# Kernel optimization log

Hardware: AMD Instinct MI355X
Metric: run time of the kernel (lower is better)

The kernel has to match this reference:

```python
import jax, jax.numpy as jnp
import numpy as np

M_CHECKS = 256      # check nodes
DC = 16             # variables per check (check degree)
NEURONS = M_CHECKS * DC  # 4096 Tanner-graph edges
BATCH = 1024
EPS = 1e-8


def build_mask():
    # edge id = check*DC + t ; mask[j, i] = 1 iff same check, different variable
    block = np.ones((DC, DC), np.float32) - np.eye(DC, dtype=np.float32)
    return jnp.asarray(np.kron(np.eye(M_CHECKS, dtype=np.float32), block))


def setup_inputs() -> dict:
    key = jax.random.key(0)
    k1, k2 = jax.random.split(key)
    # tanh-domain variable-to-check messages, |x| < ~1 (keeps exp(sum log|x|) stable)
    x = 0.25 * jax.random.normal(k1, (BATCH, NEURONS), dtype=jnp.float32)
    mask = build_mask()
    # learned weights initialized near 1 (weighted-BP init)
    even_weights = 1.0 + 0.02 * jax.random.normal(k2, (NEURONS, NEURONS), dtype=jnp.float32)
    return {"x": x, "even_weights": even_weights, "w_even2odd_mask": mask}


def reference(x, even_weights, w_even2odd_mask):
    log_abs_x = jnp.log(jnp.abs(x) + EPS)                       # [B, E]
    x_b = 0.5 - 0.5 * jnp.sign(x)                               # hard bits
    syndrome = jnp.mod(x_b @ w_even2odd_mask, 2.0)              # [B, E]
    bipolar_syndrome = 1.0 - 2.0 * syndrome
    log_abs_x_tanner = log_abs_x @ (w_even2odd_mask * even_weights)
    even_prod_messages = bipolar_syndrome * jnp.exp(log_abs_x_tanner)
    return jnp.log((1.0 + even_prod_messages + EPS) / (1.0 - even_prod_messages + EPS))
```

## Files before the change

kernel.cpp:

```cpp
#include <hip/hip_runtime.h>


constexpr int M_CHECKS = 256;
constexpr int DC = 16;
constexpr int NEURONS = M_CHECKS * DC;
constexpr int BATCH = 1024;
constexpr float EPS = 1e-8f;

constexpr int CB = 16;
constexpr int BB = 16;
constexpr int BS4 = 65;

__global__ __launch_bounds__(256) void even_layer_kernel(
    const float* __restrict__ x,
    const float* __restrict__ w,
    float* __restrict__ out)
{
    __shared__ float4 Wsh[CB * BS4];

    const int tid = (int)threadIdx.x;
    const int cb  = (int)blockIdx.x & 15;
    const int bb  = (int)blockIdx.x >> 4;

    {
        const int cl = tid >> 4;
        const int j  = tid & 15;
        const int c  = cb * CB + cl;
        const float* src = w + (size_t)(c * DC + j) * NEURONS + (size_t)(c * DC);
        #pragma unroll
        for (int k = 0; k < 4; ++k) {
            float4 v = *(const float4*)(src + 4 * k);
            if ((j >> 2) == k) {
                if ((j & 3) == 0) v.x = 0.0f;
                else if ((j & 3) == 1) v.y = 0.0f;
                else if ((j & 3) == 2) v.z = 0.0f;
                else v.w = 0.0f;
            }
            Wsh[cl * BS4 + j * 4 + k] = v;
        }
    }
    __syncthreads();

    const int bi = tid >> 4;
    const int ci = tid & 15;
    const int b  = bb * BB + bi;
    const int c  = cb * CB + ci;

    const float* xp = x + (size_t)b * NEURONS + (size_t)(c * DC);

    float la[DC];
    int sbits = 0;

    #define LOADPROC(XV, J)                                   \
        { const float xv_ = (XV);                             \
          la[J] = logf(fabsf(xv_) + EPS);                     \
          if (xv_ < 0.0f) sbits |= (1 << (J)); }

    #pragma unroll
    for (int k = 0; k < 4; ++k) {
        const float4 v = *(const float4*)(xp + 4 * k);
        LOADPROC(v.x, 4 * k + 0)
        LOADPROC(v.y, 4 * k + 1)
        LOADPROC(v.z, 4 * k + 2)
        LOADPROC(v.w, 4 * k + 3)
    }
    const int sall = __popc(sbits) & 1;

    float acc[DC];
    #pragma unroll
    for (int i = 0; i < DC; ++i) acc[i] = 0.0f;

    const int wbase = ci * BS4;
    #pragma unroll
    for (int j = 0; j < DC; ++j) {
        const float lj = la[j];
        const float4 w0 = Wsh[wbase + j * 4 + 0];
        const float4 w1 = Wsh[wbase + j * 4 + 1];
        const float4 w2 = Wsh[wbase + j * 4 + 2];
        const float4 w3 = Wsh[wbase + j * 4 + 3];
        acc[0]  = fmaf(lj, w0.x, acc[0]);
        acc[1]  = fmaf(lj, w0.y, acc[1]);
        acc[2]  = fmaf(lj, w0.z, acc[2]);
        acc[3]  = fmaf(lj, w0.w, acc[3]);
        acc[4]  = fmaf(lj, w1.x, acc[4]);
        acc[5]  = fmaf(lj, w1.y, acc[5]);
        acc[6]  = fmaf(lj, w1.z, acc[6]);
        acc[7]  = fmaf(lj, w1.w, acc[7]);
        acc[8]  = fmaf(lj, w2.x, acc[8]);
        acc[9]  = fmaf(lj, w2.y, acc[9]);
        acc[10] = fmaf(lj, w2.z, acc[10]);
        acc[11] = fmaf(lj, w2.w, acc[11]);
        acc[12] = fmaf(lj, w3.x, acc[12]);
        acc[13] = fmaf(lj, w3.y, acc[13]);
        acc[14] = fmaf(lj, w3.z, acc[14]);
        acc[15] = fmaf(lj, w3.w, acc[15]);
    }

    float* op = out + (size_t)b * NEURONS + (size_t)(c * DC);

    #define EPI(RCOMP, I)                                                   \
        { const float e_ = expf(acc[I]);                                    \
          const int par_ = sall ^ ((sbits >> (I)) & 1);                     \
          const float even_ = par_ ? -e_ : e_;                              \
          RCOMP = logf((1.0f + even_ + EPS) / (1.0f - even_ + EPS)); }

    #pragma unroll
    for (int k = 0; k < 4; ++k) {
        float4 r;
        EPI(r.x, 4 * k + 0)
        EPI(r.y, 4 * k + 1)
        EPI(r.z, 4 * k + 2)
        EPI(r.w, 4 * k + 3)
        *(float4*)(op + 4 * k) = r;
    }

    #undef LOADPROC
    #undef EPI
}

extern "C" void kernel_launch(void* const* d_in, const int* in_sizes, int n_in,
                              void* d_out, int out_size, void* d_ws, size_t ws_size,
                              hipStream_t stream) {
    const float* x = (const float*)d_in[0];
    const float* w = (const float*)d_in[1];
    float* out = (float*)d_out;

    dim3 grid((BATCH / BB) * (M_CHECKS / CB));
    dim3 block(256);
    hipLaunchKernelGGL(even_layer_kernel, grid, block, 0, stream, x, w, out);
}
```

Before: 17.81 us.

## Split each check-batch task across two threads with shared log-magnitude staging

```diff
diff --git a/kernel.cpp b/kernel.cpp
--- a/kernel.cpp
+++ b/kernel.cpp
@@ -8,104 +8,98 @@
 constexpr float EPS = 1e-8f;
 
 constexpr int CB = 16;
-constexpr int BB = 16;
+constexpr int BB = 8;
+constexpr int TASKS = CB * BB;
 constexpr int BS4 = 65;
 
-__global__ __launch_bounds__(256) void even_layer_kernel(
+__global__ __launch_bounds__(256, 6) void even_layer_kernel(
     const float* __restrict__ x,
     const float* __restrict__ w,
     float* __restrict__ out)
 {
     __shared__ float4 Wsh[CB * BS4];
+    __shared__ float  la_t[DC][TASKS + 1];
+    __shared__ int    msk_sh[2][TASKS + 2];
 
     const int tid = (int)threadIdx.x;
     const int cb  = (int)blockIdx.x & 15;
     const int bb  = (int)blockIdx.x >> 4;
 
+    const int task = tid >> 1;
+    const int h    = tid & 1;
+    const int bi   = task >> 4;
+    const int ci   = task & 15;
+    const int b    = bb * BB + bi;
+    const int c    = cb * CB + ci;
+
+    const float* xp = x + (size_t)b * NEURONS + (size_t)(c * DC + h * 8);
+    const float4 v0 = *(const float4*)(xp);
+    const float4 v1 = *(const float4*)(xp + 4);
+
     {
         const int cl = tid >> 4;
         const int j  = tid & 15;
-        const int c  = cb * CB + cl;
-        const float* src = w + (size_t)(c * DC + j) * NEURONS + (size_t)(c * DC);
+        const int cc = cb * CB + cl;
+        const float* src = w + (size_t)(cc * DC + j) * NEURONS + (size_t)(cc * DC);
         #pragma unroll
         for (int k = 0; k < 4; ++k) {
-            float4 v = *(const float4*)(src + 4 * k);
+            float4 wv = *(const float4*)(src + 4 * k);
             if ((j >> 2) == k) {
-                if ((j & 3) == 0) v.x = 0.0f;
-                else if ((j & 3) == 1) v.y = 0.0f;
-                else if ((j & 3) == 2) v.z = 0.0f;
-                else v.w = 0.0f;
+                if ((j & 3) == 0) wv.x = 0.0f;
+                else if ((j & 3) == 1) wv.y = 0.0f;
+                else if ((j & 3) == 2) wv.z = 0.0f;
+                else wv.w = 0.0f;
             }
-            Wsh[cl * BS4 + j * 4 + k] = v;
+            Wsh[cl * BS4 + j * 4 + k] = wv;
         }
+    }
+
+    {
+        const float xv[8] = {v0.x, v0.y, v0.z, v0.w, v1.x, v1.y, v1.z, v1.w};
+        int m8 = 0;
+        #pragma unroll
+        for (int jj = 0; jj < 8; ++jj) {
+            const float lv = logf(fabsf(xv[jj]) + EPS);
+            if (xv[jj] < 0.0f) m8 |= (1 << jj);
+            la_t[h * 8 + jj][task] = lv;
+        }
+        msk_sh[h][task] = m8;
     }
     __syncthreads();
 
-    const int bi = tid >> 4;
-    const int ci = tid & 15;
-    const int b  = bb * BB + bi;
-    const int c  = cb * CB + ci;
+    const int sbits = msk_sh[0][task] | (msk_sh[1][task] << 8);
+    const int sall  = __popc(sbits) & 1;
 
-    const float* xp = x + (size_t)b * NEURONS + (size_t)(c * DC);
+    float acc[8];
+    #pragma unroll
+    for (int i = 0; i < 8; ++i) acc[i] = 0.0f;
 
-    float la[DC];
-    int sbits = 0;
-
-    #define LOADPROC(XV, J)                                   \
-        { const float xv_ = (XV);                             \
-          la[J] = logf(fabsf(xv_) + EPS);                     \
-          if (xv_ < 0.0f) sbits |= (1 << (J)); }
-
-    #pragma unroll
-    for (int k = 0; k < 4; ++k) {
-        const float4 v = *(const float4*)(xp + 4 * k);
-        LOADPROC(v.x, 4 * k + 0)
-        LOADPROC(v.y, 4 * k + 1)
-        LOADPROC(v.z, 4 * k + 2)
-        LOADPROC(v.w, 4 * k + 3)
-    }
-    const int sall = __popc(sbits) & 1;
-
-    float acc[DC];
-    #pragma unroll
-    for (int i = 0; i < DC; ++i) acc[i] = 0.0f;
-
-    const int wbase = ci * BS4;
+    const int wbase = ci * BS4 + h * 2;
     #pragma unroll
     for (int j = 0; j < DC; ++j) {
-        const float lj = la[j];
-        const float4 w0 = Wsh[wbase + j * 4 + 0];
-        const float4 w1 = Wsh[wbase + j * 4 + 1];
-        const float4 w2 = Wsh[wbase + j * 4 + 2];
-        const float4 w3 = Wsh[wbase + j * 4 + 3];
-        acc[0]  = fmaf(lj, w0.x, acc[0]);
-        acc[1]  = fmaf(lj, w0.y, acc[1]);
-        acc[2]  = fmaf(lj, w0.z, acc[2]);
-        acc[3]  = fmaf(lj, w0.w, acc[3]);
-        acc[4]  = fmaf(lj, w1.x, acc[4]);
-        acc[5]  = fmaf(lj, w1.y, acc[5]);
-        acc[6]  = fmaf(lj, w1.z, acc[6]);
-        acc[7]  = fmaf(lj, w1.w, acc[7]);
-        acc[8]  = fmaf(lj, w2.x, acc[8]);
-        acc[9]  = fmaf(lj, w2.y, acc[9]);
-        acc[10] = fmaf(lj, w2.z, acc[10]);
-        acc[11] = fmaf(lj, w2.w, acc[11]);
-        acc[12] = fmaf(lj, w3.x, acc[12]);
-        acc[13] = fmaf(lj, w3.y, acc[13]);
-        acc[14] = fmaf(lj, w3.z, acc[14]);
-        acc[15] = fmaf(lj, w3.w, acc[15]);
+        const float lj = la_t[j][task];
+        const float4 wlo = Wsh[wbase + j * 4];
+        const float4 whi = Wsh[wbase + j * 4 + 1];
+        acc[0] = fmaf(lj, wlo.x, acc[0]);
+        acc[1] = fmaf(lj, wlo.y, acc[1]);
+        acc[2] = fmaf(lj, wlo.z, acc[2]);
+        acc[3] = fmaf(lj, wlo.w, acc[3]);
+        acc[4] = fmaf(lj, whi.x, acc[4]);
+        acc[5] = fmaf(lj, whi.y, acc[5]);
+        acc[6] = fmaf(lj, whi.z, acc[6]);
+        acc[7] = fmaf(lj, whi.w, acc[7]);
     }
 
-    float* op = out + (size_t)b * NEURONS + (size_t)(c * DC);
+    float* op = out + (size_t)b * NEURONS + (size_t)(c * DC + h * 8);
 
     #define EPI(RCOMP, I)                                                   \
         { const float e_ = expf(acc[I]);                                    \
-          const int par_ = sall ^ ((sbits >> (I)) & 1);                     \
+          const int par_ = sall ^ ((sbits >> (h * 8 + (I))) & 1);           \
           const float even_ = par_ ? -e_ : e_;                              \
           RCOMP = logf((1.0f + even_ + EPS) / (1.0f - even_ + EPS)); }
 
     #pragma unroll
-    for (int k = 0; k < 4; ++k) {
+    for (int k = 0; k < 2; ++k) {
         float4 r;
         EPI(r.x, 4 * k + 0)
         EPI(r.y, 4 * k + 1)
@@ -113,8 +107,6 @@
         EPI(r.w, 4 * k + 3)
         *(float4*)(op + 4 * k) = r;
     }
-
-    #undef LOADPROC
     #undef EPI
 }
 
@@ -126,6 +118,6 @@
     float* out = (float*)d_out;
 
     dim3 grid((BATCH / BB) * (M_CHECKS / CB));
-    dim3 block(256);
+    dim3 block(2 * TASKS);
     hipLaunchKernelGGL(even_layer_kernel, grid, block, 0, stream, x, w, out);
 }
```

After: 19.10 us. 1.07x slower.

## Process two batch tiles per block and prefetch x before weight staging

Applied to the files above, without the earlier changes.

```diff
diff --git a/kernel.cpp b/kernel.cpp
--- a/kernel.cpp
+++ b/kernel.cpp
@@ -9,75 +9,24 @@
 
 constexpr int CB = 16;
 constexpr int BB = 16;
+constexpr int SETS = 2;
 constexpr int BS4 = 65;
 
-__global__ __launch_bounds__(256) void even_layer_kernel(
-    const float* __restrict__ x,
-    const float* __restrict__ w,
-    float* __restrict__ out)
+__device__ __forceinline__ void matvec_epi_store(
+    const float4* __restrict__ wrow,
+    const float la[DC], const int sbits, float* __restrict__ op)
 {
-    __shared__ float4 Wsh[CB * BS4];
-
-    const int tid = (int)threadIdx.x;
-    const int cb  = (int)blockIdx.x & 15;
-    const int bb  = (int)blockIdx.x >> 4;
-
-    {
-        const int cl = tid >> 4;
-        const int j  = tid & 15;
-        const int c  = cb * CB + cl;
-        const float* src = w + (size_t)(c * DC + j) * NEURONS + (size_t)(c * DC);
-        #pragma unroll
-        for (int k = 0; k < 4; ++k) {
-            float4 v = *(const float4*)(src + 4 * k);
-            if ((j >> 2) == k) {
-                if ((j & 3) == 0) v.x = 0.0f;
-                else if ((j & 3) == 1) v.y = 0.0f;
-                else if ((j & 3) == 2) v.z = 0.0f;
-                else v.w = 0.0f;
-            }
-            Wsh[cl * BS4 + j * 4 + k] = v;
-        }
-    }
-    __syncthreads();
-
-    const int bi = tid >> 4;
-    const int ci = tid & 15;
-    const int b  = bb * BB + bi;
-    const int c  = cb * CB + ci;
-
-    const float* xp = x + (size_t)b * NEURONS + (size_t)(c * DC);
-
-    float la[DC];
-    int sbits = 0;
-
-    #define LOADPROC(XV, J)                                   \
-        { const float xv_ = (XV);                             \
-          la[J] = logf(fabsf(xv_) + EPS);                     \
-          if (xv_ < 0.0f) sbits |= (1 << (J)); }
-
-    #pragma unroll
-    for (int k = 0; k < 4; ++k) {
-        const float4 v = *(const float4*)(xp + 4 * k);
-        LOADPROC(v.x, 4 * k + 0)
-        LOADPROC(v.y, 4 * k + 1)
-        LOADPROC(v.z, 4 * k + 2)
-        LOADPROC(v.w, 4 * k + 3)
-    }
-    const int sall = __popc(sbits) & 1;
-
     float acc[DC];
     #pragma unroll
     for (int i = 0; i < DC; ++i) acc[i] = 0.0f;
 
-    const int wbase = ci * BS4;
     #pragma unroll
     for (int j = 0; j < DC; ++j) {
         const float lj = la[j];
-        const float4 w0 = Wsh[wbase + j * 4 + 0];
-        const float4 w1 = Wsh[wbase + j * 4 + 1];
-        const float4 w2 = Wsh[wbase + j * 4 + 2];
-        const float4 w3 = Wsh[wbase + j * 4 + 3];
+        const float4 w0 = wrow[j * 4 + 0];
+        const float4 w1 = wrow[j * 4 + 1];
+        const float4 w2 = wrow[j * 4 + 2];
+        const float4 w3 = wrow[j * 4 + 3];
         acc[0]  = fmaf(lj, w0.x, acc[0]);
         acc[1]  = fmaf(lj, w0.y, acc[1]);
         acc[2]  = fmaf(lj, w0.z, acc[2]);
@@ -96,7 +45,7 @@
         acc[15] = fmaf(lj, w3.w, acc[15]);
     }
 
-    float* op = out + (size_t)b * NEURONS + (size_t)(c * DC);
+    const int sall = __popc(sbits) & 1;
 
     #define EPI(RCOMP, I)                                                   \
         { const float e_ = expf(acc[I]);                                    \
@@ -113,9 +62,85 @@
         EPI(r.w, 4 * k + 3)
         *(float4*)(op + 4 * k) = r;
     }
+    #undef EPI
+}
 
-    #undef LOADPROC
-    #undef EPI
+__device__ __forceinline__ void log_abs_pack(
+    const float4 xv[4], float la[DC], int& sbits)
+{
+    const float xs[16] = {xv[0].x, xv[0].y, xv[0].z, xv[0].w,
+                          xv[1].x, xv[1].y, xv[1].z, xv[1].w,
+                          xv[2].x, xv[2].y, xv[2].z, xv[2].w,
+                          xv[3].x, xv[3].y, xv[3].z, xv[3].w};
+    sbits = 0;
+    #pragma unroll
+    for (int j = 0; j < DC; ++j) {
+        la[j] = logf(fabsf(xs[j]) + EPS);
+        if (xs[j] < 0.0f) sbits |= (1 << j);
+    }
+}
+
+__global__ __launch_bounds__(256) void even_layer_kernel(
+    const float* __restrict__ x,
+    const float* __restrict__ w,
+    float* __restrict__ out)
+{
+    __shared__ float4 Wsh[CB * BS4];
+
+    const int tid = (int)threadIdx.x;
+    const int cb  = (int)blockIdx.x & 15;
+    const int bg  = (int)blockIdx.x >> 4;
+
+    const int bi = tid >> 4;
+    const int ci = tid & 15;
+    const int b0 = bg * (SETS * BB) + bi;
+    const int b1 = b0 + BB;
+    const int c  = cb * CB + ci;
+
+    const float* xp0 = x + (size_t)b0 * NEURONS + (size_t)(c * DC);
+    const float* xp1 = x + (size_t)b1 * NEURONS + (size_t)(c * DC);
+
+    float4 xv0[4];
+    #pragma unroll
+    for (int k = 0; k < 4; ++k) xv0[k] = *(const float4*)(xp0 + 4 * k);
+
+    const int cl = tid >> 4;
+    const int jr = tid & 15;
+    const int cc = cb * CB + cl;
+    const float* wsrc = w + (size_t)(cc * DC + jr) * NEURONS + (size_t)(cc * DC);
+    float4 wreg[4];
+    #pragma unroll
+    for (int k = 0; k < 4; ++k) wreg[k] = *(const float4*)(wsrc + 4 * k);
+
+    float la0[DC]; int sb0;
+    log_abs_pack(xv0, la0, sb0);
+
+    #pragma unroll
+    for (int k = 0; k < 4; ++k) {
+        float4 wv = wreg[k];
+        if ((jr >> 2) == k) {
+            if ((jr & 3) == 0) wv.x = 0.0f;
+            else if ((jr & 3) == 1) wv.y = 0.0f;
+            else if ((jr & 3) == 2) wv.z = 0.0f;
+            else wv.w = 0.0f;
+        }
+        Wsh[cl * BS4 + jr * 4 + k] = wv;
+    }
+
+    float4 xv1[4];
+    #pragma unroll
+    for (int k = 0; k < 4; ++k) xv1[k] = *(const float4*)(xp1 + 4 * k);
+
+    __syncthreads();
+
+    const float4* wrow = &Wsh[ci * BS4];
+    matvec_epi_store(wrow, la0, sb0,
+                     out + (size_t)b0 * NEURONS + (size_t)(c * DC));
+
+    float la1[DC]; int sb1;
+    log_abs_pack(xv1, la1, sb1);
+    matvec_epi_store(wrow, la1, sb1,
+                     out + (size_t)b1 * NEURONS + (size_t)(c * DC));
 }
 
 extern "C" void kernel_launch(void* const* d_in, const int* in_sizes, int n_in,
@@ -125,7 +150,7 @@
     const float* w = (const float*)d_in[1];
     float* out = (float*)d_out;
 
-    dim3 grid((BATCH / BB) * (M_CHECKS / CB));
+    dim3 grid((BATCH / (SETS * BB)) * (M_CHECKS / CB));
     dim3 block(256);
     hipLaunchKernelGGL(even_layer_kernel, grid, block, 0, stream, x, w, out);
 }
```

Result: slower. 24.16 us (+35.7%).
